# Kernel tuning notes

Measured on AMD Instinct MI355X. Metric: run time of the kernel, lower is better.

Reference implementation:

```python
import jax, jax.numpy as jnp
import numpy as np

BITS = 4
MAXQ = 15           # 2**BITS - 1
PACK = 32 // BITS   # 8 nibbles per int32
GROUP = 128         # quantization group size along in_features


def _unpack_rows(packed, rows):
    """Unpack int32-packed 4-bit values along axis 0. packed: [Kp, N] -> [rows, N]."""
    shifts = jnp.arange(0, 32, BITS, dtype=jnp.int32)            # [PACK]
    u = (packed[:, None, :] >> shifts[None, :, None]) & MAXQ    # [Kp, PACK, N]
    return u.reshape(-1, packed.shape[1])[:rows]


def _unpack_cols(packed, cols):
    """Unpack int32-packed 4-bit values along axis 1. packed: [G, Np] -> [G, cols]."""
    shifts = jnp.arange(0, 32, BITS, dtype=jnp.int32)            # [PACK]
    u = (packed[:, :, None] >> shifts[None, None, :]) & MAXQ    # [G, Np, PACK]
    return u.reshape(packed.shape[0], -1)[:, :cols]


def setup_inputs() -> dict:
    key = jax.random.key(0)
    k1, k2, k3, k4, k5 = jax.random.split(key, 5)
    K, N = 4096, 11008
    x = jax.random.normal(k1, (4, 2048, K), dtype=jnp.float32)
    qweight = jax.random.randint(k2, (K // PACK, N), 0, 2**31 - 1, dtype=jnp.int32)
    scales = jax.random.uniform(k3, (K // GROUP, N), dtype=jnp.float32)
    qzeros = jax.random.randint(k4, (K // GROUP, (N + PACK - 1) // PACK), 0, 2**31 - 1, dtype=jnp.int32)
    bias = jax.random.normal(k5, (N,), dtype=jnp.float32)
    return {"x": x, "qweight": qweight, "scales": scales, "qzeros": qzeros, "bias": bias}


def reference(x, qweight, scales, qzeros, bias):
    K = x.shape[-1]
    N = scales.shape[1]
    qw = _unpack_rows(qweight, K)            # [K, N] int in [0, 15]
    qz = _unpack_cols(qzeros, N) + 1         # [G, N] int in [1, 16] (+1 per get_unpacked_params)
    s = jnp.repeat(scales, GROUP, axis=0)    # [K, N]  groupwise -> per-row
    z = jnp.repeat(qz, GROUP, axis=0)        # [K, N]
    W = (qw - z).astype(x.dtype) * s         # dequantized weight [K, N]
    out = jnp.matmul(x, W) + bias
    return out.astype(x.dtype)
```

## Files before the change

### kernel.cpp

```cpp
#include <hip/hip_runtime.h>
#include <hip/hip_bf16.h>
#include <stdint.h>

typedef __attribute__((ext_vector_type(4))) float f32x4;
typedef __attribute__((ext_vector_type(8))) short bf16x8;
typedef __attribute__((ext_vector_type(8))) unsigned short ushort8;
typedef __attribute__((ext_vector_type(4))) unsigned short ushort4v;

__device__ __forceinline__ unsigned short f2bf(float f) {
    union { float f; unsigned int u; } v; v.f = f;
    unsigned int u = v.u;
    u += 0x7FFFu + ((u >> 16) & 1u);
    return (unsigned short)(u >> 16);
}

__device__ __forceinline__ int swz(int row, int k) {
    return (row * 64 + k) ^ ((row & 7) << 3);
}

__device__ __forceinline__ void gld16(const void* g, void* l) {
    __builtin_amdgcn_global_load_lds(
        (const __attribute__((address_space(1))) unsigned int*)g,
        (__attribute__((address_space(3))) unsigned int*)l,
        16, 0, 0);
}

__global__ __launch_bounds__(256)
void cvt_x(const float* __restrict__ X, unsigned short* __restrict__ Xb, long long n8) {
    long long i0 = (long long)blockIdx.x * 256 + threadIdx.x;
    long long stride = (long long)gridDim.x * 256;
    for (long long i = i0; i < n8; i += stride) {
        const float4* p = reinterpret_cast<const float4*>(X + i * 8);
        float4 a = p[0], b = p[1];
        ushort8 o;
        o[0] = f2bf(a.x); o[1] = f2bf(a.y); o[2] = f2bf(a.z); o[3] = f2bf(a.w);
        o[4] = f2bf(b.x); o[5] = f2bf(b.y); o[6] = f2bf(b.z); o[7] = f2bf(b.w);
        *reinterpret_cast<ushort8*>(Xb + i * 8) = o;
    }
}

__global__ __launch_bounds__(256)
void deq_w(const int* __restrict__ QW, const float* __restrict__ SC,
           const int* __restrict__ QZ, unsigned short* __restrict__ WT,
           int N, int K) {
    const int ntiles = N >> 6;
    const int nb = blockIdx.x % ntiles;
    const int kb = blockIdx.x / ntiles;
    const int n0 = nb * 64, kp0 = kb * 64;
    const int t = threadIdx.x;
    #pragma unroll
    for (int w = 0; w < 16; ++w) {
        const int p = t + 256 * w;
        const int kpo = p & 63, ni = p >> 6;
        const int n = n0 + ni, kp = kp0 + kpo;
        const int g = kp >> 4;
        const float s = SC[(size_t)g * N + n];
        const int zq = ((QZ[(size_t)g * (N >> 3) + (n >> 3)] >> ((n & 7) * 4)) & 15) + 1;
        const float zb = -(float)zq * s;
        const unsigned int q = (unsigned int)QW[(size_t)kp * N + n];
        ushort8 o;
        #pragma unroll
        for (int j = 0; j < 8; ++j)
            o[j] = f2bf(fmaf((float)((q >> (4 * j)) & 15u), s, zb));
        *reinterpret_cast<ushort8*>(&WT[(size_t)n * K + kp * 8]) = o;
    }
}

template<int KC, int NC>
__global__ __launch_bounds__(512, 2)
void qgemm_256(const unsigned short* __restrict__ Xb, const unsigned short* __restrict__ WT,
               const float* __restrict__ BIAS, float* __restrict__ OUT, int M) {
    __shared__ __align__(16) unsigned short S[65536];

    int id = blockIdx.x;
    const int nwg = gridDim.x;
    if ((nwg & 7) == 0) id = (id & 7) * (nwg >> 3) + (id >> 3);

    constexpr int ntn = NC >> 8;
    const int bm = (id / ntn) << 8;
    const int bn = (id % ntn) << 8;
    const int tid = threadIdx.x;
    const int lane = tid & 63;
    const int wid = tid >> 6;
    const int wm = (wid >> 2) * 64;
    const int wn = (wid & 3) * 32;
    const int lr = lane & 15;
    const int lk = (lane >> 4) * 8;

    const int xr  = (lr & 7) << 3;
    const int lo0 = lk ^ xr;
    const int lo1 = (32 + lk) ^ xr;
    const int lrow = lr * 64;

    f32x4 acc[8][4] = {};
    constexpr int nk = KC >> 6;

    const int srow = tid >> 3;
    const int scol = ((tid & 7) ^ (srow & 7)) << 3;
    const unsigned short* gA[2] = { Xb + (size_t)(bm + srow) * KC + scol,
                                    Xb + (size_t)(bm + 128 + srow) * KC + scol };
    const unsigned short* gB[2] = { WT + (size_t)(bn + srow) * KC + scol,
                                    WT + (size_t)(bn + 128 + srow) * KC + scol };

    auto stage = [&](int buf, int tt, int kind, int half) {
        const unsigned short* g = (kind ? gB[half] : gA[half]) + (size_t)tt * 64;
        unsigned short* lb = S + (kind ? 32768 : 0) + buf * 16384 + half * 8192 + tid * 8;
        gld16(g, lb);
        gld16(g + (size_t)64 * KC, lb + 4096);
    };

    bf16x8 aL[4][2], aH[4][2], bL[2][2], bH[2][2];

    auto loadA = [&](bf16x8 (&dst)[4][2], const unsigned short* Sa, int rbase) {
        const unsigned short* p = Sa + rbase * 64 + lrow;
        #pragma unroll
        for (int i = 0; i < 4; ++i) {
            dst[i][0] = *reinterpret_cast<const bf16x8*>(p + i * 1024 + lo0);
            dst[i][1] = *reinterpret_cast<const bf16x8*>(p + i * 1024 + lo1);
        }
    };
    auto loadB = [&](bf16x8 (&dst)[2][2], const unsigned short* Sb, int rbase) {
        const unsigned short* p = Sb + rbase * 64 + lrow;
        #pragma unroll
        for (int j = 0; j < 2; ++j) {
            dst[j][0] = *reinterpret_cast<const bf16x8*>(p + j * 1024 + lo0);
            dst[j][1] = *reinterpret_cast<const bf16x8*>(p + j * 1024 + lo1);
        }
    };
    auto quad = [&](bf16x8 (&A)[4][2], bf16x8 (&B)[2][2], int mi0, int nj0) {
        __builtin_amdgcn_s_setprio(1);
        #pragma unroll
        for (int kk = 0; kk < 2; ++kk)
            #pragma unroll
            for (int i = 0; i < 4; ++i)
                #pragma unroll
                for (int j = 0; j < 2; ++j)
                    acc[mi0 + i][nj0 + j] = __builtin_amdgcn_mfma_f32_16x16x32_bf16(
                        A[i][kk], B[j][kk], acc[mi0 + i][nj0 + j], 0, 0, 0);
        __builtin_amdgcn_s_setprio(0);
    };

    const unsigned short* Sa0 = S;
    const unsigned short* Sa1 = S + 16384;
    const unsigned short* Sb0 = S + 32768;
    const unsigned short* Sb1 = S + 49152;

    stage(0, 0, 0, 0); stage(0, 0, 0, 1);
    stage(0, 0, 1, 0); stage(0, 0, 1, 1);
    stage(1, 1, 0, 0); stage(1, 1, 1, 1); stage(1, 1, 0, 1);
    asm volatile("s_waitcnt vmcnt(6)" ::: "memory");

    auto tile = [&](int t, int c, const unsigned short* Sa, const unsigned short* Sb) {
        __builtin_amdgcn_s_barrier();
        if (t + 1 < nk) stage(c ^ 1, t + 1, 1, 0);
        loadA(aL, Sa, wm);
        loadB(bL, Sb, wn);
        quad(aL, bL, 0, 0);

        __builtin_amdgcn_s_barrier();
        if (t + 2 < nk) stage(c, t + 2, 0, 0);
        loadB(bH, Sb, 128 + wn);
        quad(aL, bH, 0, 2);

        __builtin_amdgcn_s_barrier();
        if (t + 2 < nk) stage(c, t + 2, 1, 1);
        loadA(aH, Sa, 128 + wm);
        quad(aH, bL, 4, 0);

        __builtin_amdgcn_s_barrier();
        if (t + 2 < nk) {
            stage(c, t + 2, 0, 1);
            asm volatile("s_waitcnt vmcnt(6)" ::: "memory");
        } else {
            asm volatile("s_waitcnt vmcnt(0)" ::: "memory");
        }
        quad(aH, bH, 4, 2);
    };

    for (int t = 0; t < nk; t += 2) {
        tile(t,     0, Sa0, Sb0);
        tile(t + 1, 1, Sa1, Sb1);
    }

    #pragma unroll
    for (int mi = 0; mi < 8; ++mi) {
        const int row = bm + wm + (mi & 3) * 16 + ((mi >> 2) ? 128 : 0) + (lane >> 4) * 4;
        #pragma unroll
        for (int nj = 0; nj < 4; ++nj) {
            const int col = bn + wn + (nj & 1) * 16 + ((nj >> 1) ? 128 : 0) + lr;
            const float b = BIAS[col];
            #pragma unroll
            for (int r = 0; r < 4; ++r)
                OUT[(size_t)(row + r) * NC + col] = acc[mi][nj][r] + b;
        }
    }
}

__global__ __launch_bounds__(256, 2)
void qgemm_ws(const unsigned short* __restrict__ Xb, const unsigned short* __restrict__ WT,
              const float* __restrict__ BIAS, float* __restrict__ OUT,
              int M, int N, int K) {
    __shared__ __align__(16) unsigned short As[2][128 * 64];
    __shared__ __align__(16) unsigned short Bs[2][128 * 64];

    const int ntn = N >> 7;
    const int bm = (blockIdx.x / ntn) * 128;
    const int bn = (blockIdx.x % ntn) * 128;
    const int tid = threadIdx.x;
    const int lane = tid & 63;
    const int wave = tid >> 6;
    const int wm = (wave >> 1) * 64, wn = (wave & 1) * 64;
    const int lr = lane & 15, lk = (lane >> 4) * 8;

    f32x4 acc[4][4] = {};
    const int nk = K >> 6;

    auto stage = [&](int buf, int t) {
        const int k0 = t * 64;
        #pragma unroll
        for (int p = 0; p < 4; ++p) {
            const int slot = p * 256 + tid;
            const int row = slot >> 3, c = slot & 7;
            const int gk = k0 + ((c ^ (row & 7)) << 3);
            gld16(Xb + (size_t)(bm + row) * K + gk, &As[buf][slot * 8]);
            gld16(WT + (size_t)(bn + row) * K + gk, &Bs[buf][slot * 8]);
        }
    };

    auto compute = [&](int buf) {
        #pragma unroll
        for (int kk = 0; kk < 2; ++kk) {
            bf16x8 af[4], bfr[4];
            #pragma unroll
            for (int i = 0; i < 4; ++i) {
                af[i]  = *reinterpret_cast<const bf16x8*>(&As[buf][swz(wm + i * 16 + lr, kk * 32 + lk)]);
                bfr[i] = *reinterpret_cast<const bf16x8*>(&Bs[buf][swz(wn + i * 16 + lr, kk * 32 + lk)]);
            }
            #pragma unroll
            for (int i = 0; i < 4; ++i)
                #pragma unroll
                for (int j = 0; j < 4; ++j)
                    acc[i][j] = __builtin_amdgcn_mfma_f32_16x16x32_bf16(af[i], bfr[j], acc[i][j], 0, 0, 0);
        }
    };

    stage(0, 0);
    __syncthreads();
    int cur = 0;
    for (int t = 0; t < nk; ++t) {
        if (t + 1 < nk) stage(cur ^ 1, t + 1);
        compute(cur);
        __syncthreads();
        cur ^= 1;
    }

    #pragma unroll
    for (int i = 0; i < 4; ++i) {
        #pragma unroll
        for (int j = 0; j < 4; ++j) {
            const int col = bn + wn + j * 16 + lr;
            const float b = BIAS[col];
            #pragma unroll
            for (int r = 0; r < 4; ++r) {
                const int row = bm + wm + i * 16 + (lane >> 4) * 4 + r;
                OUT[(size_t)row * N + col] = acc[i][j][r] + b;
            }
        }
    }
}

__global__ __launch_bounds__(256, 2)
void qgemm_fb(const float* __restrict__ X, const int* __restrict__ QW,
              const float* __restrict__ SC, const int* __restrict__ QZ,
              const float* __restrict__ BIAS, float* __restrict__ OUT,
              int M, int N, int K) {
    __shared__ __align__(16) unsigned short As[2][128 * 64];
    __shared__ __align__(16) unsigned short Bs[2][128 * 64];

    const int ntn = N / 128;
    const int bm = (blockIdx.x / ntn) * 128;
    const int bn = (blockIdx.x % ntn) * 128;
    const int tid  = threadIdx.x;
    const int lane = tid & 63;
    const int wave = tid >> 6;
    const int wm = (wave >> 1) * 64, wn = (wave & 1) * 64;
    const int lr = lane & 15, lk = (lane >> 4) * 8;
    const int a_c4 = tid & 15, a_r0 = tid >> 4;
    const int b_n  = tid & 127, b_k0 = tid >> 7;

    f32x4 acc[4][4] = {};
    float4 va[8];
    unsigned int wb[4];
    float sc_s = 0.f, sc_zb = 0.f;
    const int nk = K / 64;

    auto gload = [&](int t) {
        const int k0 = t * 64;
        #pragma unroll
        for (int p = 0; p < 8; ++p)
            va[p] = *reinterpret_cast<const float4*>(X + (size_t)(bm + a_r0 + p * 16) * K + k0 + a_c4 * 4);
        const int g  = k0 >> 7;
        const int gn = bn + b_n;
        sc_s = SC[(size_t)g * N + gn];
        const int zq = ((QZ[(size_t)g * (N >> 3) + (gn >> 3)] >> ((gn & 7) * 4)) & 15) + 1;
        sc_zb = -(float)zq * sc_s;
        #pragma unroll
        for (int p = 0; p < 4; ++p)
            wb[p] = (unsigned int)QW[(size_t)(t * 8 + b_k0 + p * 2) * N + gn];
    };

    auto lwrite = [&](int buf) {
        #pragma unroll
        for (int p = 0; p < 8; ++p) {
            const int row = a_r0 + p * 16;
            ushort4v b;
            b.x = f2bf(va[p].x); b.y = f2bf(va[p].y);
            b.z = f2bf(va[p].z); b.w = f2bf(va[p].w);
            *reinterpret_cast<ushort4v*>(&As[buf][swz(row, a_c4 * 4)]) = b;
        }
        #pragma unroll
        for (int p = 0; p < 4; ++p) {
            const int ko = b_k0 + p * 2;
            ushort8 o;
            #pragma unroll
            for (int j = 0; j < 8; ++j)
                o[j] = f2bf(fmaf((float)((wb[p] >> (4 * j)) & 15u), sc_s, sc_zb));
            *reinterpret_cast<ushort8*>(&Bs[buf][swz(b_n, ko * 8)]) = o;
        }
    };

    auto compute = [&](int buf) {
        #pragma unroll
        for (int kk = 0; kk < 2; ++kk) {
            bf16x8 af[4], bfr[4];
            #pragma unroll
            for (int i = 0; i < 4; ++i) {
                af[i]  = *reinterpret_cast<const bf16x8*>(&As[buf][swz(wm + i * 16 + lr, kk * 32 + lk)]);
                bfr[i] = *reinterpret_cast<const bf16x8*>(&Bs[buf][swz(wn + i * 16 + lr, kk * 32 + lk)]);
            }
            #pragma unroll
            for (int i = 0; i < 4; ++i)
                #pragma unroll
                for (int j = 0; j < 4; ++j)
                    acc[i][j] = __builtin_amdgcn_mfma_f32_16x16x32_bf16(af[i], bfr[j], acc[i][j], 0, 0, 0);
        }
    };

    gload(0); lwrite(0);
    __syncthreads();
    for (int t = 0; t < nk; ++t) {
        if (t + 1 < nk) gload(t + 1);
        compute(t & 1);
        if (t + 1 < nk) lwrite((t + 1) & 1);
        __syncthreads();
    }

    #pragma unroll
    for (int i = 0; i < 4; ++i) {
        #pragma unroll
        for (int j = 0; j < 4; ++j) {
            const int col = bn + wn + j * 16 + lr;
            const float b = BIAS[col];
            #pragma unroll
            for (int r = 0; r < 4; ++r) {
                const int row = bm + wm + i * 16 + (lane >> 4) * 4 + r;
                OUT[(size_t)row * N + col] = acc[i][j][r] + b;
            }
        }
    }
}

extern "C" void kernel_launch(void* const* d_in, const int* in_sizes, int n_in,
                              void* d_out, int out_size, void* d_ws, size_t ws_size,
                              hipStream_t stream) {
    const float* X    = (const float*)d_in[0];
    const int*   QW   = (const int*)d_in[1];
    const float* SC   = (const float*)d_in[2];
    const int*   QZ   = (const int*)d_in[3];
    const float* BIAS = (const float*)d_in[4];
    float* OUT = (float*)d_out;

    const int N = in_sizes[4];
    const long long qwsz = in_sizes[1];
    const int K = (int)(qwsz * 8 / N);
    const int M = in_sizes[0] / K;

    const size_t xb_bytes = (size_t)M * K * 2;
    const size_t wt_bytes = (size_t)N * K * 2;

    if (ws_size >= xb_bytes + wt_bytes) {
        unsigned short* Xb = (unsigned short*)d_ws;
        unsigned short* WT = Xb + (size_t)M * K;

        cvt_x<<<2048, 256, 0, stream>>>(X, Xb, (long long)M * K / 8);
        deq_w<<<(N >> 6) * (K / 512), 256, 0, stream>>>(QW, SC, QZ, WT, N, K);

        if (K == 4096 && N == 11008 && (M % 256) == 0) {
            qgemm_256<4096, 11008><<<(M / 256) * (11008 / 256), 512, 0, stream>>>(Xb, WT, BIAS, OUT, M);
        } else {
            qgemm_ws<<<(M / 128) * (N / 128), 256, 0, stream>>>(Xb, WT, BIAS, OUT, M, N, K);
        }
    } else {
        qgemm_fb<<<(M / 128) * (N / 128), 256, 0, stream>>>(X, QW, SC, QZ, BIAS, OUT, M, N, K);
    }
}
```

Baseline: 746.7 us.

## Use triple-buffered B-low tile to issue all next-tile loads at two-tile distance

```diff
diff --git a/kernel.cpp b/kernel.cpp
--- a/kernel.cpp
+++ b/kernel.cpp
@@ -70,7 +70,7 @@
 __global__ __launch_bounds__(512, 2)
 void qgemm_256(const unsigned short* __restrict__ Xb, const unsigned short* __restrict__ WT,
                const float* __restrict__ BIAS, float* __restrict__ OUT, int M) {
-    __shared__ __align__(16) unsigned short S[65536];
+    __shared__ __align__(16) unsigned short S[73728];
 
     int id = blockIdx.x;
     const int nwg = gridDim.x;
@@ -102,25 +102,24 @@
     const unsigned short* gB[2] = { WT + (size_t)(bn + srow) * KC + scol,
                                     WT + (size_t)(bn + 128 + srow) * KC + scol };
 
-    auto stage = [&](int buf, int tt, int kind, int half) {
-        const unsigned short* g = (kind ? gB[half] : gA[half]) + (size_t)tt * 64;
-        unsigned short* lb = S + (kind ? 32768 : 0) + buf * 16384 + half * 8192 + tid * 8;
+    auto stage2 = [&](const unsigned short* g, int ldsoff) {
+        unsigned short* lb = S + ldsoff + tid * 8;
         gld16(g, lb);
         gld16(g + (size_t)64 * KC, lb + 4096);
     };
 
     bf16x8 aL[4][2], aH[4][2], bL[2][2], bH[2][2];
 
-    auto loadA = [&](bf16x8 (&dst)[4][2], const unsigned short* Sa, int rbase) {
-        const unsigned short* p = Sa + rbase * 64 + lrow;
+    auto loadA = [&](bf16x8 (&dst)[4][2], const unsigned short* base) {
+        const unsigned short* p = base + wm * 64 + lrow;
         #pragma unroll
         for (int i = 0; i < 4; ++i) {
             dst[i][0] = *reinterpret_cast<const bf16x8*>(p + i * 1024 + lo0);
             dst[i][1] = *reinterpret_cast<const bf16x8*>(p + i * 1024 + lo1);
         }
     };
-    auto loadB = [&](bf16x8 (&dst)[2][2], const unsigned short* Sb, int rbase) {
-        const unsigned short* p = Sb + rbase * 64 + lrow;
+    auto loadB = [&](bf16x8 (&dst)[2][2], const unsigned short* base) {
+        const unsigned short* p = base + wn * 64 + lrow;
         #pragma unroll
         for (int j = 0; j < 2; ++j) {
             dst[j][0] = *reinterpret_cast<const bf16x8*>(p + j * 1024 + lo0);
@@ -140,46 +139,52 @@
         __builtin_amdgcn_s_setprio(0);
     };
 
-    const unsigned short* Sa0 = S;
-    const unsigned short* Sa1 = S + 16384;
-    const unsigned short* Sb0 = S + 32768;
-    const unsigned short* Sb1 = S + 49152;
-
-    stage(0, 0, 0, 0); stage(0, 0, 0, 1);
-    stage(0, 0, 1, 0); stage(0, 0, 1, 1);
-    stage(1, 1, 0, 0); stage(1, 1, 1, 1); stage(1, 1, 0, 1);
-    asm volatile("s_waitcnt vmcnt(6)" ::: "memory");
-
-    auto tile = [&](int t, int c, const unsigned short* Sa, const unsigned short* Sb) {
+    stage2(gA[0], 0);            stage2(gB[0], 49152);
+    stage2(gB[1], 32768);        stage2(gA[1], 8192);
+    stage2(gA[0] + 64, 16384);   stage2(gB[0] + 64, 49152 + 8192);
+    stage2(gB[1] + 64, 32768 + 8192); stage2(gA[1] + 64, 16384 + 8192);
+    asm volatile("s_waitcnt vmcnt(8)" ::: "memory");
+
+    auto tile = [&](int t, int c, int brd, int bst) {
+        const unsigned short* Sa  = S + c * 16384;
+        const unsigned short* SbH = S + 32768 + c * 8192;
+        const unsigned short* SbL = S + 49152 + brd * 8192;
+
         __builtin_amdgcn_s_barrier();
-        if (t + 1 < nk) stage(c ^ 1, t + 1, 1, 0);
-        loadA(aL, Sa, wm);
-        loadB(bL, Sb, wn);
+        loadA(aL, Sa);
+        loadB(bL, SbL);
         quad(aL, bL, 0, 0);
-
-        __builtin_amdgcn_s_barrier();
-        if (t + 2 < nk) stage(c, t + 2, 0, 0);
-        loadB(bH, Sb, 128 + wn);
-        quad(aL, bH, 0, 2);
-
-        __builtin_amdgcn_s_barrier();
-        if (t + 2 < nk) stage(c, t + 2, 1, 1);
-        loadA(aH, Sa, 128 + wm);
-        quad(aH, bL, 4, 0);
 
         __builtin_amdgcn_s_barrier();
         if (t + 2 < nk) {
-            stage(c, t + 2, 0, 1);
-            asm volatile("s_waitcnt vmcnt(6)" ::: "memory");
+            stage2(gA[0] + (size_t)(t + 2) * 64, c * 16384);
+            stage2(gB[0] + (size_t)(t + 2) * 64, 49152 + bst * 8192);
+        }
+        loadB(bH, SbH);
+        quad(aL, bH, 0, 2);
+
+        __builtin_amdgcn_s_barrier();
+        if (t + 2 < nk) stage2(gB[1] + (size_t)(t + 2) * 64, 32768 + c * 8192);
+        loadA(aH, Sa + 8192);
+        quad(aH, bL, 4, 0);
+
+        __builtin_amdgcn_s_barrier();
+        if (t + 2 < nk) {
+            stage2(gA[1] + (size_t)(t + 2) * 64, c * 16384 + 8192);
+            asm volatile("s_waitcnt vmcnt(8)" ::: "memory");
         } else {
             asm volatile("s_waitcnt vmcnt(0)" ::: "memory");
         }
         quad(aH, bH, 4, 2);
     };
 
-    for (int t = 0; t < nk; t += 2) {
-        tile(t,     0, Sa0, Sb0);
-        tile(t + 1, 1, Sa1, Sb1);
+    for (int t = 0; t < nk; t += 6) {
+        tile(t,     0, 0, 2);
+        if (t + 1 < nk) tile(t + 1, 1, 1, 0);
+        if (t + 2 < nk) tile(t + 2, 0, 2, 1);
+        if (t + 3 < nk) tile(t + 3, 1, 0, 2);
+        if (t + 4 < nk) tile(t + 4, 0, 1, 0);
+        if (t + 5 < nk) tile(t + 5, 1, 2, 1);
     }
 
     #pragma unroll
```

Result: no change. 757.3 us (+1.4%).

## Fuse x conversion and weight dequant into one prep kernel; restructure GEMM loop

Applied to the files above, without the earlier changes.

```diff
diff --git a/kernel.cpp b/kernel.cpp
--- a/kernel.cpp
+++ b/kernel.cpp
@@ -23,6 +23,48 @@
         (const __attribute__((address_space(1))) unsigned int*)g,
         (__attribute__((address_space(3))) unsigned int*)l,
         16, 0, 0);
+}
+
+__global__ __launch_bounds__(256)
+void prep(const float* __restrict__ X, const int* __restrict__ QW,
+          const float* __restrict__ SC, const int* __restrict__ QZ,
+          unsigned short* __restrict__ Xb, unsigned short* __restrict__ WT,
+          int N, int K, long long n8, int deqB) {
+    const int bid = blockIdx.x;
+    const int t = threadIdx.x;
+    if (bid < deqB) {
+        const int ntiles = N >> 6;
+        const int nb = bid % ntiles;
+        const int kb = bid / ntiles;
+        const int n0 = nb * 64, kp0 = kb * 64;
+        #pragma unroll
+        for (int w = 0; w < 16; ++w) {
+            const int p = t + 256 * w;
+            const int kpo = p & 63, ni = p >> 6;
+            const int n = n0 + ni, kp = kp0 + kpo;
+            const int g = kp >> 4;
+            const float s = SC[(size_t)g * N + n];
+            const int zq = ((QZ[(size_t)g * (N >> 3) + (n >> 3)] >> ((n & 7) * 4)) & 15) + 1;
+            const float zb = -(float)zq * s;
+            const unsigned int q = (unsigned int)QW[(size_t)kp * N + n];
+            ushort8 o;
+            #pragma unroll
+            for (int j = 0; j < 8; ++j)
+                o[j] = f2bf(fmaf((float)((q >> (4 * j)) & 15u), s, zb));
+            *reinterpret_cast<ushort8*>(&WT[(size_t)n * K + kp * 8]) = o;
+        }
+    } else {
+        long long i0 = (long long)(bid - deqB) * 256 + t;
+        long long stride = (long long)(gridDim.x - deqB) * 256;
+        for (long long i = i0; i < n8; i += stride) {
+            const float4* p = reinterpret_cast<const float4*>(X + i * 8);
+            float4 a = p[0], b = p[1];
+            ushort8 o;
+            o[0] = f2bf(a.x); o[1] = f2bf(a.y); o[2] = f2bf(a.z); o[3] = f2bf(a.w);
+            o[4] = f2bf(b.x); o[5] = f2bf(b.y); o[6] = f2bf(b.z); o[7] = f2bf(b.w);
+            *reinterpret_cast<ushort8*>(Xb + i * 8) = o;
+        }
+    }
 }
 
 __global__ __launch_bounds__(256)
@@ -140,34 +182,34 @@
         __builtin_amdgcn_s_setprio(0);
     };
 
-    const unsigned short* Sa0 = S;
-    const unsigned short* Sa1 = S + 16384;
-    const unsigned short* Sb0 = S + 32768;
-    const unsigned short* Sb1 = S + 49152;
-
     stage(0, 0, 0, 0); stage(0, 0, 0, 1);
     stage(0, 0, 1, 0); stage(0, 0, 1, 1);
     stage(1, 1, 0, 0); stage(1, 1, 1, 1); stage(1, 1, 0, 1);
     asm volatile("s_waitcnt vmcnt(6)" ::: "memory");
 
-    auto tile = [&](int t, int c, const unsigned short* Sa, const unsigned short* Sb) {
+    for (int t = 0; t < nk; ++t) {
+        const int c = t & 1;
+        const unsigned short* Sa = S + c * 16384;
+        const unsigned short* Sb = S + 32768 + c * 16384;
+
+        if (t + 1 < nk) stage(c ^ 1, t + 1, 1, 0);
+
         __builtin_amdgcn_s_barrier();
-        if (t + 1 < nk) stage(c ^ 1, t + 1, 1, 0);
         loadA(aL, Sa, wm);
         loadB(bL, Sb, wn);
         quad(aL, bL, 0, 0);
-
         __builtin_amdgcn_s_barrier();
+
         if (t + 2 < nk) stage(c, t + 2, 0, 0);
         loadB(bH, Sb, 128 + wn);
         quad(aL, bH, 0, 2);
-
         __builtin_amdgcn_s_barrier();
+
         if (t + 2 < nk) stage(c, t + 2, 1, 1);
         loadA(aH, Sa, 128 + wm);
         quad(aH, bL, 4, 0);
-
         __builtin_amdgcn_s_barrier();
+
         if (t + 2 < nk) {
             stage(c, t + 2, 0, 1);
             asm volatile("s_waitcnt vmcnt(6)" ::: "memory");
@@ -175,11 +217,6 @@
             asm volatile("s_waitcnt vmcnt(0)" ::: "memory");
         }
         quad(aH, bH, 4, 2);
-    };
-
-    for (int t = 0; t < nk; t += 2) {
-        tile(t,     0, Sa0, Sb0);
-        tile(t + 1, 1, Sa1, Sb1);
     }
 
     #pragma unroll
@@ -392,12 +429,14 @@
         unsigned short* Xb = (unsigned short*)d_ws;
         unsigned short* WT = Xb + (size_t)M * K;
 
-        cvt_x<<<2048, 256, 0, stream>>>(X, Xb, (long long)M * K / 8);
-        deq_w<<<(N >> 6) * (K / 512), 256, 0, stream>>>(QW, SC, QZ, WT, N, K);
-
         if (K == 4096 && N == 11008 && (M % 256) == 0) {
+            const int deqB = (N >> 6) * (K / 512);
+            prep<<<deqB + 2048, 256, 0, stream>>>(X, QW, SC, QZ, Xb, WT,
+                                                  N, K, (long long)M * K / 8, deqB);
             qgemm_256<4096, 11008><<<(M / 256) * (11008 / 256), 512, 0, stream>>>(Xb, WT, BIAS, OUT, M);
         } else {
+            cvt_x<<<2048, 256, 0, stream>>>(X, Xb, (long long)M * K / 8);
+            deq_w<<<(N >> 6) * (K / 512), 256, 0, stream>>>(QW, SC, QZ, WT, N, K);
             qgemm_ws<<<(M / 128) * (N / 128), 256, 0, stream>>>(Xb, WT, BIAS, OUT, M, N, K);
         }
     } else {
```

Result: no change. 746.7 us (-0.0%).
